# Kernel optimization log

Hardware: AMD Instinct MI355X
Metric: run time of the kernel (lower is better)

Reference implementation:

```python
import jax, jax.numpy as jnp
import numpy as np

N_NODES = 100000
MAX_DEG = 128
NODE_DIM = 256
BATCH = 4096
NUM_SAMPLES = 32


def setup_inputs() -> dict:
    key = jax.random.key(0)
    k1, k2, k3, k4 = jax.random.split(key, 4)
    adj_info = jax.random.randint(k1, (N_NODES, MAX_DEG), 0, N_NODES, dtype=jnp.int32)
    features = jax.random.normal(k2, (N_NODES, NODE_DIM), dtype=jnp.float32)
    ids = jax.random.randint(k3, (BATCH,), 0, N_NODES, dtype=jnp.int32)
    W = jax.random.normal(k4, (NODE_DIM, NODE_DIM), dtype=jnp.float32) * 0.05
    b = jnp.zeros((NODE_DIM,), jnp.float32)
    return {"adj_info": adj_info, "features": features, "ids": ids,
            "W": W, "b": b, "num_samples": NUM_SAMPLES}


def reference(adj_info, features, ids, W, b, num_samples):
    # adj_info: [n_nodes, neig_num] int32; features: [n_nodes, D]
    V = ids.shape[0]
    neig_num = adj_info.shape[1]
    group_dim = neig_num // num_samples
    n_keep = group_dim * num_samples

    adj_lists = adj_info[ids][:, :n_keep]          # [V, N] gather
    v_f = features[ids]                            # [V, D]
    n_f = features[adj_lists]                      # [V, N, D] gather

    # linear sampler branch: dense(v_f) then matmul against neighbor features
    l = v_f @ W + b                                # [V, D]
    scores = jax.nn.relu(jnp.einsum('vd,vnd->vn', l, n_f))  # [V, N]

    # grouped argmin: neighbor index = s*group_dim + argmin within group
    scores = scores.reshape(V, num_samples, group_dim)
    idx_y = jnp.argmin(scores, axis=-1).astype(jnp.int32)   # [V, S]
    idx_y = idx_y + (jnp.arange(num_samples, dtype=jnp.int32) * group_dim)[None, :]

    sel = jnp.take_along_axis(adj_lists, idx_y, axis=1)     # [V, S]

    # count non-dummy neighbors (dummy id = n_nodes - 1)
    is_dummy = sel == (adj_info.shape[0] - 1)
    adj_lists_numnz = jnp.sum(jnp.where(is_dummy, 0.0, 1.0), axis=1)  # [V]
    att_lists = jnp.ones((V, num_samples), jnp.float32)
    dummy_ = adj_lists_numnz
    return sel, att_lists, adj_lists_numnz, dummy_
```

## Files before the change

kernel.cpp:

```cpp
#include <hip/hip_runtime.h>
#include <hip/hip_bf16.h>


constexpr int D        = 256;
constexpr int V        = 4096;
constexpr int MAXDEG   = 128;
constexpr int S        = 32;
constexpr int DUMMY_ID = 99999;

constexpr int OFF_SEL  = 0;
constexpr int OFF_ATT  = V * S;
constexpr int OFF_NNZ  = 2 * V * S;
constexpr int OFF_DMY  = 2 * V * S + V;

__device__ __forceinline__ float bf16_round_f32(float f) {
    unsigned int u = __float_as_uint(f);
    u += 0x7FFFu + ((u >> 16) & 1u);
    u &= 0xFFFF0000u;
    return __uint_as_float(u);
}

__global__ __launch_bounds__(256) void fused_k(
    const int* __restrict__ adj, const float* __restrict__ features,
    const int* __restrict__ ids, const float* __restrict__ W,
    const float* __restrict__ bias, float* __restrict__ out)
{
    const int v    = blockIdx.x;
    const int tid  = threadIdx.x;
    const int lane = tid & 63;
    const int wave = tid >> 6;

    __shared__ float  vf[D];
    __shared__ double lsh[D];
    __shared__ int cnt;
    if (tid == 0) cnt = 0;

    const int node = ids[v];
    vf[tid] = features[(size_t)node * D + tid];

    if (tid < S) out[OFF_ATT + v * S + tid] = 1.0f;
    __syncthreads();

    double a0 = (double)bias[tid], a1 = 0.0, a2 = 0.0, a3 = 0.0;
    #pragma unroll 4
    for (int d = 0; d < D; d += 4) {
        a0 = fma((double)vf[d    ], (double)W[(d    ) * D + tid], a0);
        a1 = fma((double)vf[d + 1], (double)W[(d + 1) * D + tid], a1);
        a2 = fma((double)vf[d + 2], (double)W[(d + 2) * D + tid], a2);
        a3 = fma((double)vf[d + 3], (double)W[(d + 3) * D + tid], a3);
    }
    lsh[tid] = (a0 + a1) + (a2 + a3);
    __syncthreads();

    const double2 l01 = *reinterpret_cast<const double2*>(&lsh[lane * 4]);
    const double2 l23 = *reinterpret_cast<const double2*>(&lsh[lane * 4 + 2]);
    const int* arow = adj + (size_t)node * MAXDEG + wave * 32;

    int localcnt = 0;

    #pragma unroll
    for (int g = 0; g < 8; ++g) {
        const int4 nb4 = *reinterpret_cast<const int4*>(arow + g * 4);

        const float4 f0 = *reinterpret_cast<const float4*>(features + (size_t)nb4.x * D + lane * 4);
        const float4 f1 = *reinterpret_cast<const float4*>(features + (size_t)nb4.y * D + lane * 4);
        const float4 f2 = *reinterpret_cast<const float4*>(features + (size_t)nb4.z * D + lane * 4);
        const float4 f3 = *reinterpret_cast<const float4*>(features + (size_t)nb4.w * D + lane * 4);

        double p0 = fma(l01.x, (double)f0.x, fma(l01.y, (double)f0.y,
                    fma(l23.x, (double)f0.z, l23.y * (double)f0.w)));
        double p1 = fma(l01.x, (double)f1.x, fma(l01.y, (double)f1.y,
                    fma(l23.x, (double)f1.z, l23.y * (double)f1.w)));
        double p2 = fma(l01.x, (double)f2.x, fma(l01.y, (double)f2.y,
                    fma(l23.x, (double)f2.z, l23.y * (double)f2.w)));
        double p3 = fma(l01.x, (double)f3.x, fma(l01.y, (double)f3.y,
                    fma(l23.x, (double)f3.z, l23.y * (double)f3.w)));

        #pragma unroll
        for (int off = 32; off; off >>= 1) {
            p0 += __shfl_xor(p0, off);
            p1 += __shfl_xor(p1, off);
            p2 += __shfl_xor(p2, off);
            p3 += __shfl_xor(p3, off);
        }

        const double s0 = fmax(p0, 0.0);
        const double s1 = fmax(p1, 0.0);
        const double s2 = fmax(p2, 0.0);
        const double s3 = fmax(p3, 0.0);

        double bs = s0; int selid = nb4.x;
        if (s1 < bs) { bs = s1; selid = nb4.y; }
        if (s2 < bs) { bs = s2; selid = nb4.z; }
        if (s3 < bs) { bs = s3; selid = nb4.w; }

        if (lane == 0) {
            out[OFF_SEL + v * S + wave * 8 + g] = bf16_round_f32((float)selid);
            if (selid != DUMMY_ID) ++localcnt;
        }
    }

    if (lane == 0 && localcnt) atomicAdd(&cnt, localcnt);
    __syncthreads();
    if (tid == 0) {
        const float c = (float)cnt;
        out[OFF_NNZ + v] = c;
        out[OFF_DMY + v] = c;
    }
}

extern "C" void kernel_launch(void* const* d_in, const int* in_sizes, int n_in,
                              void* d_out, int out_size, void* d_ws, size_t ws_size,
                              hipStream_t stream)
{
    const int*   adj      = (const int*)d_in[0];
    const float* features = (const float*)d_in[1];
    const int*   ids      = (const int*)d_in[2];
    const float* W        = (const float*)d_in[3];
    const float* bias     = (const float*)d_in[4];
    (void)d_ws; (void)ws_size;

    float* out = (float*)d_out;

    fused_k<<<V, 256, 0, stream>>>(adj, features, ids, W, bias, out);
}
```

Before: 255.2 us.

## Split each wavefront into four 16-lane groups, one neighbor per group

Each wavefront now handles four neighbors at once, one per group of 16 lanes, instead of reducing four neighbors across all 64 lanes. The projected vector is stored in a transposed shared-memory layout so each lane reads matching elements. The dot-product reduction shrinks to 4 shuffle steps per neighbor, and a shuffle-based argmin with index tie-break picks the winner across groups. The change also adds an occupancy hint to launch bounds and lowers unroll factors, which may cut register pressure at the cost of less instruction-level parallelism on the loads.

New measurement: 315.6 us. +23.7%, slower.

```diff
diff --git a/kernel.cpp b/kernel.cpp
--- a/kernel.cpp
+++ b/kernel.cpp
@@ -20,83 +20,93 @@
     return __uint_as_float(u);
 }
 
-__global__ __launch_bounds__(256) void fused_k(
+__global__ __launch_bounds__(256, 8) void fused_k(
     const int* __restrict__ adj, const float* __restrict__ features,
     const int* __restrict__ ids, const float* __restrict__ W,
     const float* __restrict__ bias, float* __restrict__ out)
 {
-    const int v    = blockIdx.x;
     const int tid  = threadIdx.x;
     const int lane = tid & 63;
     const int wave = tid >> 6;
+    const int v    = blockIdx.x;
 
     __shared__ float  vf[D];
-    __shared__ double lsh[D];
-    __shared__ int cnt;
+    __shared__ double lshT[D];
+    __shared__ int    cnt;
     if (tid == 0) cnt = 0;
 
     const int node = ids[v];
     vf[tid] = features[(size_t)node * D + tid];
-
     if (tid < S) out[OFF_ATT + v * S + tid] = 1.0f;
     __syncthreads();
 
-    double a0 = (double)bias[tid], a1 = 0.0, a2 = 0.0, a3 = 0.0;
-    #pragma unroll 4
-    for (int d = 0; d < D; d += 4) {
-        a0 = fma((double)vf[d    ], (double)W[(d    ) * D + tid], a0);
-        a1 = fma((double)vf[d + 1], (double)W[(d + 1) * D + tid], a1);
-        a2 = fma((double)vf[d + 2], (double)W[(d + 2) * D + tid], a2);
-        a3 = fma((double)vf[d + 3], (double)W[(d + 3) * D + tid], a3);
+    {
+        double a0 = (double)bias[tid], a1 = 0.0, a2 = 0.0, a3 = 0.0;
+        #pragma unroll 2
+        for (int d = 0; d < D; d += 4) {
+            a0 = fma((double)vf[d    ], (double)W[(d    ) * D + tid], a0);
+            a1 = fma((double)vf[d + 1], (double)W[(d + 1) * D + tid], a1);
+            a2 = fma((double)vf[d + 2], (double)W[(d + 2) * D + tid], a2);
+            a3 = fma((double)vf[d + 3], (double)W[(d + 3) * D + tid], a3);
+        }
+        const double lval = (a0 + a1) + (a2 + a3);
+        const int c = tid >> 6, rem = tid & 63;
+        lshT[(c << 6) + ((rem & 3) << 4) + (rem >> 2)] = lval;
     }
-    lsh[tid] = (a0 + a1) + (a2 + a3);
     __syncthreads();
 
-    const double2 l01 = *reinterpret_cast<const double2*>(&lsh[lane * 4]);
-    const double2 l23 = *reinterpret_cast<const double2*>(&lsh[lane * 4 + 2]);
-    const int* arow = adj + (size_t)node * MAXDEG + wave * 32;
+    const int l16 = lane & 15;
+    const int g   = lane >> 4;
+    const int* arow = adj + (size_t)node * MAXDEG;
 
     int localcnt = 0;
 
-    #pragma unroll
-    for (int g = 0; g < 8; ++g) {
-        const int4 nb4 = *reinterpret_cast<const int4*>(arow + g * 4);
+    #pragma unroll 2
+    for (int s8 = 0; s8 < 8; ++s8) {
+        const int s  = wave * 8 + s8;
+        const int nb = arow[4 * s + g];
+        const float* r = features + (size_t)nb * D + (l16 << 2);
 
-        const float4 f0 = *reinterpret_cast<const float4*>(features + (size_t)nb4.x * D + lane * 4);
-        const float4 f1 = *reinterpret_cast<const float4*>(features + (size_t)nb4.y * D + lane * 4);
-        const float4 f2 = *reinterpret_cast<const float4*>(features + (size_t)nb4.z * D + lane * 4);
-        const float4 f3 = *reinterpret_cast<const float4*>(features + (size_t)nb4.w * D + lane * 4);
+        const float4 x0 = *reinterpret_cast<const float4*>(r);
+        const float4 x1 = *reinterpret_cast<const float4*>(r + 64);
+        const float4 x2 = *reinterpret_cast<const float4*>(r + 128);
+        const float4 x3 = *reinterpret_cast<const float4*>(r + 192);
 
-        double p0 = fma(l01.x, (double)f0.x, fma(l01.y, (double)f0.y,
-                    fma(l23.x, (double)f0.z, l23.y * (double)f0.w)));
-        double p1 = fma(l01.x, (double)f1.x, fma(l01.y, (double)f1.y,
-                    fma(l23.x, (double)f1.z, l23.y * (double)f1.w)));
-        double p2 = fma(l01.x, (double)f2.x, fma(l01.y, (double)f2.y,
-                    fma(l23.x, (double)f2.z, l23.y * (double)f2.w)));
-        double p3 = fma(l01.x, (double)f3.x, fma(l01.y, (double)f3.y,
-                    fma(l23.x, (double)f3.z, l23.y * (double)f3.w)));
+        double pa = 0.0, pb = 0.0, pc = 0.0, pd = 0.0;
+        pa = fma(lshT[      l16      ], (double)x0.x, pa);
+        pb = fma(lshT[      l16 + 16 ], (double)x0.y, pb);
+        pc = fma(lshT[      l16 + 32 ], (double)x0.z, pc);
+        pd = fma(lshT[      l16 + 48 ], (double)x0.w, pd);
+        pa = fma(lshT[ 64 + l16      ], (double)x1.x, pa);
+        pb = fma(lshT[ 64 + l16 + 16 ], (double)x1.y, pb);
+        pc = fma(lshT[ 64 + l16 + 32 ], (double)x1.z, pc);
+        pd = fma(lshT[ 64 + l16 + 48 ], (double)x1.w, pd);
+        pa = fma(lshT[128 + l16      ], (double)x2.x, pa);
+        pb = fma(lshT[128 + l16 + 16 ], (double)x2.y, pb);
+        pc = fma(lshT[128 + l16 + 32 ], (double)x2.z, pc);
+        pd = fma(lshT[128 + l16 + 48 ], (double)x2.w, pd);
+        pa = fma(lshT[192 + l16      ], (double)x3.x, pa);
+        pb = fma(lshT[192 + l16 + 16 ], (double)x3.y, pb);
+        pc = fma(lshT[192 + l16 + 32 ], (double)x3.z, pc);
+        pd = fma(lshT[192 + l16 + 48 ], (double)x3.w, pd);
 
+        double t = (pa + pb) + (pc + pd);
         #pragma unroll
-        for (int off = 32; off; off >>= 1) {
-            p0 += __shfl_xor(p0, off);
-            p1 += __shfl_xor(p1, off);
-            p2 += __shfl_xor(p2, off);
-            p3 += __shfl_xor(p3, off);
+        for (int off = 1; off < 16; off <<= 1) t += __shfl_xor(t, off);
+        double bs = fmax(t, 0.0);
+
+        int bp = g, bid = nb;
+        #pragma unroll
+        for (int off = 16; off < 64; off <<= 1) {
+            const double so = __shfl_xor(bs,  off);
+            const int    po = __shfl_xor(bp,  off);
+            const int    io = __shfl_xor(bid, off);
+            if (so < bs || (so == bs && po < bp)) { bs = so; bp = po; bid = io; }
         }
 
-        const double s0 = fmax(p0, 0.0);
-        const double s1 = fmax(p1, 0.0);
-        const double s2 = fmax(p2, 0.0);
-        const double s3 = fmax(p3, 0.0);
-
-        double bs = s0; int selid = nb4.x;
-        if (s1 < bs) { bs = s1; selid = nb4.y; }
-        if (s2 < bs) { bs = s2; selid = nb4.z; }
-        if (s3 < bs) { bs = s3; selid = nb4.w; }
-
         if (lane == 0) {
-            out[OFF_SEL + v * S + wave * 8 + g] = bf16_round_f32((float)selid);
-            if (selid != DUMMY_ID) ++localcnt;
+            out[OFF_SEL + v * S + s] = bf16_round_f32((float)bid);
+            if (bid != DUMMY_ID) ++localcnt;
         }
     }
 
```
